# Optimization experiments

Measured on AMD Instinct MI355X. Metric: run time of the kernel, lower is better.

## Reference

```python
import jax, jax.numpy as jnp
import numpy as np

NUM_HEADS = 16
D_K = 64
BATCH_SIZE = 64
NUM_EDGES = 32768


def setup_inputs() -> dict:
    key = jax.random.key(0)
    k1, k2, k3, k4 = jax.random.split(key, 4)
    global_query = jax.random.normal(k1, (NUM_HEADS, BATCH_SIZE, D_K), dtype=jnp.float32)
    local_key = jax.random.normal(k2, (NUM_HEADS, NUM_EDGES, D_K), dtype=jnp.float32)
    local_value = jax.random.normal(k3, (NUM_HEADS, NUM_EDGES, D_K), dtype=jnp.float32)
    batch = jnp.sort(jax.random.randint(k4, (NUM_EDGES,), 0, BATCH_SIZE, dtype=jnp.int64))
    return {"global_query": global_query, "local_key": local_key,
            "local_value": local_value, "batch": batch}


def reference(global_query, local_key, local_value, batch):
    # global_query: [h, b, d]; local_key/value: [h, e, d]; batch: [e] segment ids
    num_heads, batch_size, d_k = global_query.shape
    # seg[b, e] = True iff edge e belongs to graph b
    seg = batch[None, :] == jnp.arange(batch_size, dtype=batch.dtype)[:, None]  # [b, e]
    # NOTE: original module does NOT scale by sqrt(d_k) despite its name
    scores = jnp.einsum('hbd,hed->hbe', global_query, local_key)  # [h, b, e]
    # per-segment softmax: out-of-segment entries get -inf -> exactly 0 weight,
    # matching the original which only softmaxes over edges with batch == i
    masked = jnp.where(seg[None, :, :], scores, -jnp.inf)
    attn = jax.nn.softmax(masked, axis=-1)  # [h, b, e]; zeros outside segment
    output = jnp.einsum('hbe,hed->hbd', attn, local_value)  # [h, b, d]
    return output, attn
```

## Files before the change

### kernel.cpp

```cpp
#include <hip/hip_runtime.h>
#include <math.h>

#define NH 16
#define NB 64
#define DK 64
#define NE 32768

typedef float vf4 __attribute__((ext_vector_type(4)));


__global__ void seg_bounds_kernel(const int* __restrict__ batch, int* __restrict__ bounds) {
    int e = blockIdx.x * 256 + threadIdx.x;
    if (e >= NE) return;
    int be = batch[e];
    if (e == 0) {
        for (int b = 0; b <= be; ++b) bounds[b] = 0;
    } else {
        int bp = batch[e - 1];
        for (int b = bp + 1; b <= be; ++b) bounds[b] = e;
    }
    if (e == NE - 1) {
        for (int b = be + 1; b <= NB; ++b) bounds[b] = NE;
    }
}

__global__ __launch_bounds__(256) void scores_kernel(
    const float* __restrict__ Q,
    const float* __restrict__ K,
    const int*   __restrict__ bounds,
    float* __restrict__ ksc_base,
    float* __restrict__ mstash)
{
    const int g    = blockIdx.x;
    const int task = g >> 1;
    const int half = g & 1;
    const int h    = task >> 6;
    const int b    = task & (NB - 1);
    const int tid  = threadIdx.x;
    const int wave = tid >> 6;
    const int lane = tid & 63;
    const int j    = lane >> 4;
    const int c    = lane & 15;

    const int start = bounds[b];
    const int end   = bounds[b + 1];
    const int S     = end - start;
    const int Sh    = (S + 1) >> 1;
    const int s0    = start + half * Sh;
    const int e1    = (s0 + Sh < end) ? s0 + Sh : end;

    float* ksc = ksc_base + (size_t)h * NE;

    __shared__ float qs[DK];
    __shared__ float sm[4], sl[4];
    if (tid < DK) qs[tid] = Q[((size_t)h * NB + b) * DK + tid];
    __syncthreads();

    const float4 qc = ((const float4*)qs)[c];
    const float4* K4 = (const float4*)(K + (size_t)h * NE * DK);

    float m = -INFINITY, l = 0.f;
    int e = s0 + wave * 4;

    for (; e + 115 < e1; e += 128) {
        float4 kv[8];
        #pragma unroll
        for (int u = 0; u < 8; ++u)
            kv[u] = K4[(size_t)(e + 16 * u + j) * (DK / 4) + c];
        float s[8];
        #pragma unroll
        for (int u = 0; u < 8; ++u) {
            float t = fmaf(kv[u].x, qc.x, fmaf(kv[u].y, qc.y,
                      fmaf(kv[u].z, qc.z, kv[u].w * qc.w)));
            #pragma unroll
            for (int off = 1; off < 16; off <<= 1)
                t += __shfl_xor(t, off);
            s[u] = t;
            if (c == 0) ksc[e + 16 * u + j] = t;
        }
        float mx = fmaxf(fmaxf(fmaxf(s[0], s[1]), fmaxf(s[2], s[3])),
                         fmaxf(fmaxf(s[4], s[5]), fmaxf(s[6], s[7])));
        const float nm = fmaxf(m, mx);
        float sum = 0.f;
        #pragma unroll
        for (int u = 0; u < 8; ++u) sum += __expf(s[u] - nm);
        l = l * __expf(m - nm) + sum;
        m = nm;
    }
    for (; e < e1; e += 16) {
        const int  ej    = e + j;
        const bool valid = ej < e1;
        const int  el    = valid ? ej : e1 - 1;
        const float4 kv = K4[(size_t)el * (DK / 4) + c];
        float s = fmaf(kv.x, qc.x, fmaf(kv.y, qc.y, fmaf(kv.z, qc.z, kv.w * qc.w)));
        #pragma unroll
        for (int off = 1; off < 16; off <<= 1)
            s += __shfl_xor(s, off);
        if (valid) {
            if (c == 0) ksc[ej] = s;
            float nm = fmaxf(m, s);
            l = l * __expf(m - nm) + __expf(s - nm);
            m = nm;
        }
    }

    #pragma unroll
    for (int off = 16; off < 64; off <<= 1) {
        float om = __shfl_xor(m, off);
        float ol = __shfl_xor(l, off);
        float nm = fmaxf(m, om);
        float t1 = (l  > 0.f) ? l  * __expf(m  - nm) : 0.f;
        float t2 = (ol > 0.f) ? ol * __expf(om - nm) : 0.f;
        m = nm; l = t1 + t2;
    }
    if (lane == 0) { sm[wave] = m; sl[wave] = l; }
    __syncthreads();

    if (tid == 0) {
        float M = -INFINITY;
        #pragma unroll
        for (int w = 0; w < 4; ++w) M = fmaxf(M, sm[w]);
        float L = 0.f;
        #pragma unroll
        for (int w = 0; w < 4; ++w) L += (sl[w] > 0.f) ? sl[w] * __expf(sm[w] - M) : 0.f;
        mstash[(task * 2 + half) * 2 + 0] = M;
        mstash[(task * 2 + half) * 2 + 1] = L;
    }
}

__global__ __launch_bounds__(256) void bc_kernel(
    const int*   __restrict__ batch,
    const float* __restrict__ ksc_base,
    const float* __restrict__ mstash,
    const float* __restrict__ V,
    const int*   __restrict__ bounds,
    float* __restrict__ attn,
    float* __restrict__ out)
{
    const int blk = blockIdx.x;
    const int tid = threadIdx.x;
    __shared__ float red[4][16][4];

    if ((blk & 1) == 0) {
        const int wb = blk >> 1;
        const unsigned total = (unsigned)NH * NB * (NE / 4);
        for (unsigned idx = wb * 256u + tid; idx < total; idx += 1024u * 256u) {
            const int e4 = idx & (NE / 4 - 1);
            const int bh = idx >> 13;
            const int b  = bh & (NB - 1);
            const int e0 = e4 << 2;
            const int4 bt = *(const int4*)(batch + e0);
            vf4 r = (vf4)(0.f);
            if (bt.x == b || bt.y == b || bt.z == b || bt.w == b) {
                const float m0 = mstash[bh * 4 + 0], l0 = mstash[bh * 4 + 1];
                const float m1 = mstash[bh * 4 + 2], l1 = mstash[bh * 4 + 3];
                const float M = fmaxf(m0, m1);
                float L = 0.f;
                if (l0 > 0.f) L += l0 * __expf(m0 - M);
                if (l1 > 0.f) L += l1 * __expf(m1 - M);
                const float inv = (L > 0.f) ? 1.f / L : 0.f;
                const int h = bh >> 6;
                const float4 s = *(const float4*)(ksc_base + (size_t)h * NE + e0);
                if (bt.x == b) r.x = __expf(s.x - M) * inv;
                if (bt.y == b) r.y = __expf(s.y - M) * inv;
                if (bt.z == b) r.z = __expf(s.z - M) * inv;
                if (bt.w == b) r.w = __expf(s.w - M) * inv;
            }
            *((vf4*)attn + idx) = r;
        }
    } else {
        const int task = blk >> 1;
        const int h    = task >> 6;
        const int b    = task & (NB - 1);
        const int wave = tid >> 6;
        const int lane = tid & 63;
        const int j    = lane >> 4;
        const int c    = lane & 15;

        const int start = bounds[b];
        const int end   = bounds[b + 1];

        const float m0 = mstash[task * 4 + 0], l0 = mstash[task * 4 + 1];
        const float m1 = mstash[task * 4 + 2], l1 = mstash[task * 4 + 3];
        const float M = fmaxf(m0, m1);
        float L = 0.f;
        if (l0 > 0.f) L += l0 * __expf(m0 - M);
        if (l1 > 0.f) L += l1 * __expf(m1 - M);
        const float inv = (L > 0.f) ? 1.f / L : 0.f;

        const float*  ksc = ksc_base + (size_t)h * NE;
        const float4* V4  = (const float4*)(V + (size_t)h * NE * DK);

        float4 acc = make_float4(0.f, 0.f, 0.f, 0.f);
        int e = start + wave * 4;

        for (; e + 115 < end; e += 128) {
            float4 v[8]; float p[8];
            #pragma unroll
            for (int u = 0; u < 8; ++u) {
                const int ej = e + 16 * u + j;
                p[u] = ksc[ej];
                v[u] = V4[(size_t)ej * (DK / 4) + c];
            }
            #pragma unroll
            for (int u = 0; u < 8; ++u) {
                const float pe = __expf(p[u] - M) * inv;
                acc.x = fmaf(pe, v[u].x, acc.x);
                acc.y = fmaf(pe, v[u].y, acc.y);
                acc.z = fmaf(pe, v[u].z, acc.z);
                acc.w = fmaf(pe, v[u].w, acc.w);
            }
        }
        for (; e < end; e += 16) {
            const int  ej    = e + j;
            const bool valid = ej < end;
            const int  el    = valid ? ej : end - 1;
            const float pe = valid ? __expf(ksc[ej] - M) * inv : 0.f;
            const float4 v = V4[(size_t)el * (DK / 4) + c];
            acc.x = fmaf(pe, v.x, acc.x);
            acc.y = fmaf(pe, v.y, acc.y);
            acc.z = fmaf(pe, v.z, acc.z);
            acc.w = fmaf(pe, v.w, acc.w);
        }

        #pragma unroll
        for (int off = 16; off < 64; off <<= 1) {
            acc.x += __shfl_xor(acc.x, off);
            acc.y += __shfl_xor(acc.y, off);
            acc.z += __shfl_xor(acc.z, off);
            acc.w += __shfl_xor(acc.w, off);
        }
        if (lane < 16) {
            red[wave][c][0] = acc.x;
            red[wave][c][1] = acc.y;
            red[wave][c][2] = acc.z;
            red[wave][c][3] = acc.w;
        }
        __syncthreads();
        if (tid < DK) {
            const int cc = tid >> 2, comp = tid & 3;
            float r = red[0][cc][comp] + red[1][cc][comp]
                    + red[2][cc][comp] + red[3][cc][comp];
            out[((size_t)h * NB + b) * DK + tid] = r;
        }
    }
}

extern "C" void kernel_launch(void* const* d_in, const int* in_sizes, int n_in,
                              void* d_out, int out_size, void* d_ws, size_t ws_size,
                              hipStream_t stream) {
    const float* Q     = (const float*)d_in[0];
    const float* K     = (const float*)d_in[1];
    const float* V     = (const float*)d_in[2];
    const int*   batch = (const int*)d_in[3];

    float* out  = (float*)d_out;
    float* attn = out + (size_t)NH * NB * DK;

    int*   bounds = (int*)d_ws;
    float* ksc    = (float*)d_ws + 128;
    float* mstash = ksc + (size_t)NH * NE;

    seg_bounds_kernel<<<NE / 256, 256, 0, stream>>>(batch, bounds);

    scores_kernel<<<2048, 256, 0, stream>>>(Q, K, bounds, ksc, mstash);

    bc_kernel<<<2048, 256, 0, stream>>>(batch, ksc, mstash, V, bounds, attn, out);
}
```

Before: 330.8 us.

## Fuse scores, softmax, attn write and PV into one kernel per head-segment

Merges the scores and the attn/output kernels into one kernel with one block per (head, graph), keeping each segment's scores in LDS instead of a global scratch buffer. Every block writes its full attention row, with zeros outside its segment, plus the normalized probabilities and the weighted V sum. This removes one launch and the global score round trip, and it no longer scans the batch array for the attn fill. In exchange the grid shrinks from 2048 to 1024 blocks with no split of a segment across two blocks, and segments longer than the LDS capacity fall back to recomputing the scores.

```diff
diff --git a/kernel.cpp b/kernel.cpp
--- a/kernel.cpp
+++ b/kernel.cpp
@@ -5,6 +5,7 @@
 #define NB 64
 #define DK 64
 #define NE 32768
+#define LDS_CAP 2048
 
 typedef float vf4 __attribute__((ext_vector_type(4)));
 
@@ -24,16 +25,15 @@
     }
 }
 
-__global__ __launch_bounds__(256) void scores_kernel(
+__global__ __launch_bounds__(256) void fused_kernel(
     const float* __restrict__ Q,
     const float* __restrict__ K,
+    const float* __restrict__ V,
     const int*   __restrict__ bounds,
-    float* __restrict__ ksc_base,
-    float* __restrict__ mstash)
+    float* __restrict__ out,
+    float* __restrict__ attn)
 {
-    const int g    = blockIdx.x;
-    const int task = g >> 1;
-    const int half = g & 1;
+    const int task = blockIdx.x;
     const int h    = task >> 6;
     const int b    = task & (NB - 1);
     const int tid  = threadIdx.x;
@@ -45,24 +45,25 @@
     const int start = bounds[b];
     const int end   = bounds[b + 1];
     const int S     = end - start;
-    const int Sh    = (S + 1) >> 1;
-    const int s0    = start + half * Sh;
-    const int e1    = (s0 + Sh < end) ? s0 + Sh : end;
-
-    float* ksc = ksc_base + (size_t)h * NE;
+    const bool single = (S <= LDS_CAP);
 
     __shared__ float qs[DK];
+    __shared__ float ssc[LDS_CAP];
     __shared__ float sm[4], sl[4];
+    __shared__ float bM, bInv;
+    __shared__ float red[4][16][4];
+
     if (tid < DK) qs[tid] = Q[((size_t)h * NB + b) * DK + tid];
     __syncthreads();
 
-    const float4 qc = ((const float4*)qs)[c];
-    const float4* K4 = (const float4*)(K + (size_t)h * NE * DK);
+    const float4  qc  = ((const float4*)qs)[c];
+    const float4* K4  = (const float4*)(K + (size_t)h * NE * DK);
+    const float4* V4  = (const float4*)(V + (size_t)h * NE * DK);
+    float* arow = attn + ((size_t)h * NB + b) * NE;
 
     float m = -INFINITY, l = 0.f;
-    int e = s0 + wave * 4;
-
-    for (; e + 115 < e1; e += 128) {
+    int e = start + wave * 4;
+    for (; e + 115 < end; e += 128) {
         float4 kv[8];
         #pragma unroll
         for (int u = 0; u < 8; ++u)
@@ -76,7 +77,7 @@
             for (int off = 1; off < 16; off <<= 1)
                 t += __shfl_xor(t, off);
             s[u] = t;
-            if (c == 0) ksc[e + 16 * u + j] = t;
+            if (single && c == 0) ssc[e + 16 * u + j - start] = t;
         }
         float mx = fmaxf(fmaxf(fmaxf(s[0], s[1]), fmaxf(s[2], s[3])),
                          fmaxf(fmaxf(s[4], s[5]), fmaxf(s[6], s[7])));
@@ -87,19 +88,19 @@
         l = l * __expf(m - nm) + sum;
         m = nm;
     }
-    for (; e < e1; e += 16) {
+    for (; e < end; e += 16) {
         const int  ej    = e + j;
-        const bool valid = ej < e1;
-        const int  el    = valid ? ej : e1 - 1;
+        const bool valid = ej < end;
+        const int  el    = valid ? ej : end - 1;
         const float4 kv = K4[(size_t)el * (DK / 4) + c];
-        float s = fmaf(kv.x, qc.x, fmaf(kv.y, qc.y, fmaf(kv.z, qc.z, kv.w * qc.w)));
+        float t = fmaf(kv.x, qc.x, fmaf(kv.y, qc.y, fmaf(kv.z, qc.z, kv.w * qc.w)));
         #pragma unroll
         for (int off = 1; off < 16; off <<= 1)
-            s += __shfl_xor(s, off);
+            t += __shfl_xor(t, off);
         if (valid) {
-            if (c == 0) ksc[ej] = s;
-            float nm = fmaxf(m, s);
-            l = l * __expf(m - nm) + __expf(s - nm);
+            if (single && c == 0) ssc[ej - start] = t;
+            float nm = fmaxf(m, t);
+            l = l * __expf(m - nm) + __expf(t - nm);
             m = nm;
         }
     }
@@ -115,7 +116,6 @@
     }
     if (lane == 0) { sm[wave] = m; sl[wave] = l; }
     __syncthreads();
-
     if (tid == 0) {
         float M = -INFINITY;
         #pragma unroll
@@ -123,83 +123,39 @@
         float L = 0.f;
         #pragma unroll
         for (int w = 0; w < 4; ++w) L += (sl[w] > 0.f) ? sl[w] * __expf(sm[w] - M) : 0.f;
-        mstash[(task * 2 + half) * 2 + 0] = M;
-        mstash[(task * 2 + half) * 2 + 1] = L;
-    }
-}
-
-__global__ __launch_bounds__(256) void bc_kernel(
-    const int*   __restrict__ batch,
-    const float* __restrict__ ksc_base,
-    const float* __restrict__ mstash,
-    const float* __restrict__ V,
-    const int*   __restrict__ bounds,
-    float* __restrict__ attn,
-    float* __restrict__ out)
-{
-    const int blk = blockIdx.x;
-    const int tid = threadIdx.x;
-    __shared__ float red[4][16][4];
-
-    if ((blk & 1) == 0) {
-        const int wb = blk >> 1;
-        const unsigned total = (unsigned)NH * NB * (NE / 4);
-        for (unsigned idx = wb * 256u + tid; idx < total; idx += 1024u * 256u) {
-            const int e4 = idx & (NE / 4 - 1);
-            const int bh = idx >> 13;
-            const int b  = bh & (NB - 1);
-            const int e0 = e4 << 2;
-            const int4 bt = *(const int4*)(batch + e0);
-            vf4 r = (vf4)(0.f);
-            if (bt.x == b || bt.y == b || bt.z == b || bt.w == b) {
-                const float m0 = mstash[bh * 4 + 0], l0 = mstash[bh * 4 + 1];
-                const float m1 = mstash[bh * 4 + 2], l1 = mstash[bh * 4 + 3];
-                const float M = fmaxf(m0, m1);
-                float L = 0.f;
-                if (l0 > 0.f) L += l0 * __expf(m0 - M);
-                if (l1 > 0.f) L += l1 * __expf(m1 - M);
-                const float inv = (L > 0.f) ? 1.f / L : 0.f;
-                const int h = bh >> 6;
-                const float4 s = *(const float4*)(ksc_base + (size_t)h * NE + e0);
-                if (bt.x == b) r.x = __expf(s.x - M) * inv;
-                if (bt.y == b) r.y = __expf(s.y - M) * inv;
-                if (bt.z == b) r.z = __expf(s.z - M) * inv;
-                if (bt.w == b) r.w = __expf(s.w - M) * inv;
-            }
-            *((vf4*)attn + idx) = r;
-        }
-    } else {
-        const int task = blk >> 1;
-        const int h    = task >> 6;
-        const int b    = task & (NB - 1);
-        const int wave = tid >> 6;
-        const int lane = tid & 63;
-        const int j    = lane >> 4;
-        const int c    = lane & 15;
-
-        const int start = bounds[b];
-        const int end   = bounds[b + 1];
-
-        const float m0 = mstash[task * 4 + 0], l0 = mstash[task * 4 + 1];
-        const float m1 = mstash[task * 4 + 2], l1 = mstash[task * 4 + 3];
-        const float M = fmaxf(m0, m1);
-        float L = 0.f;
-        if (l0 > 0.f) L += l0 * __expf(m0 - M);
-        if (l1 > 0.f) L += l1 * __expf(m1 - M);
-        const float inv = (L > 0.f) ? 1.f / L : 0.f;
-
-        const float*  ksc = ksc_base + (size_t)h * NE;
-        const float4* V4  = (const float4*)(V + (size_t)h * NE * DK);
-
-        float4 acc = make_float4(0.f, 0.f, 0.f, 0.f);
-        int e = start + wave * 4;
-
-        for (; e + 115 < end; e += 128) {
+        bM = M; bInv = (L > 0.f) ? 1.f / L : 0.f;
+    }
+    __syncthreads();
+    const float M   = bM;
+    const float inv = bInv;
+
+    {
+        vf4 z4 = (vf4)(0.f);
+        vf4* arow4 = (vf4*)arow;
+        const int zs = start >> 2;
+        const int ze = (end + 3) >> 2;
+        for (int i = tid; i < zs; i += 256) arow4[i] = z4;
+        for (int i = ze + tid; i < NE / 4; i += 256) arow4[i] = z4;
+        if (tid == 0) {
+            for (int p = (zs << 2); p < start; ++p) arow[p] = 0.f;
+        } else if (tid == 1) {
+            for (int p = end; p < (ze << 2); ++p) arow[p] = 0.f;
+        }
+    }
+
+    float4 acc = make_float4(0.f, 0.f, 0.f, 0.f);
+
+    if (single) {
+        for (int ep = start + tid; ep < end; ep += 256)
+            arow[ep] = __expf(ssc[ep - start] - M) * inv;
+
+        int ev = start + wave * 4;
+        for (; ev + 115 < end; ev += 128) {
             float4 v[8]; float p[8];
             #pragma unroll
             for (int u = 0; u < 8; ++u) {
-                const int ej = e + 16 * u + j;
-                p[u] = ksc[ej];
+                const int ej = ev + 16 * u + j;
+                p[u] = ssc[ej - start];
                 v[u] = V4[(size_t)ej * (DK / 4) + c];
             }
             #pragma unroll
@@ -211,38 +167,68 @@
                 acc.w = fmaf(pe, v[u].w, acc.w);
             }
         }
-        for (; e < end; e += 16) {
-            const int  ej    = e + j;
+        for (; ev < end; ev += 16) {
+            const int  ej    = ev + j;
             const bool valid = ej < end;
             const int  el    = valid ? ej : end - 1;
-            const float pe = valid ? __expf(ksc[ej] - M) * inv : 0.f;
+            const float pe = valid ? __expf(ssc[el - start] - M) * inv : 0.f;
             const float4 v = V4[(size_t)el * (DK / 4) + c];
             acc.x = fmaf(pe, v.x, acc.x);
             acc.y = fmaf(pe, v.y, acc.y);
             acc.z = fmaf(pe, v.z, acc.z);
             acc.w = fmaf(pe, v.w, acc.w);
         }
-
-        #pragma unroll
-        for (int off = 16; off < 64; off <<= 1) {
-            acc.x += __shfl_xor(acc.x, off);
-            acc.y += __shfl_xor(acc.y, off);
-            acc.z += __shfl_xor(acc.z, off);
-            acc.w += __shfl_xor(acc.w, off);
-        }
-        if (lane < 16) {
-            red[wave][c][0] = acc.x;
-            red[wave][c][1] = acc.y;
-            red[wave][c][2] = acc.z;
-            red[wave][c][3] = acc.w;
-        }
-        __syncthreads();
-        if (tid < DK) {
-            const int cc = tid >> 2, comp = tid & 3;
-            float r = red[0][cc][comp] + red[1][cc][comp]
-                    + red[2][cc][comp] + red[3][cc][comp];
-            out[((size_t)h * NB + b) * DK + tid] = r;
-        }
+    } else {
+        for (int cs = start; cs < end; cs += LDS_CAP) {
+            const int ce = (cs + LDS_CAP < end) ? cs + LDS_CAP : end;
+            __syncthreads();
+            for (int ek = cs + wave * 4; ek < ce; ek += 16) {
+                const int  ej    = ek + j;
+                const bool valid = ej < ce;
+                const int  el    = valid ? ej : ce - 1;
+                const float4 kv = K4[(size_t)el * (DK / 4) + c];
+                float t = fmaf(kv.x, qc.x, fmaf(kv.y, qc.y, fmaf(kv.z, qc.z, kv.w * qc.w)));
+                #pragma unroll
+                for (int off = 1; off < 16; off <<= 1)
+                    t += __shfl_xor(t, off);
+                if (valid && c == 0) ssc[el - cs] = t;
+            }
+            __syncthreads();
+            for (int ep = cs + tid; ep < ce; ep += 256)
+                arow[ep] = __expf(ssc[ep - cs] - M) * inv;
+            for (int ev = cs + wave * 4; ev < ce; ev += 16) {
+                const int  ej    = ev + j;
+                const bool valid = ej < ce;
+                const int  el    = valid ? ej : ce - 1;
+                const float pe = valid ? __expf(ssc[el - cs] - M) * inv : 0.f;
+                const float4 v = V4[(size_t)el * (DK / 4) + c];
+                acc.x = fmaf(pe, v.x, acc.x);
+                acc.y = fmaf(pe, v.y, acc.y);
+                acc.z = fmaf(pe, v.z, acc.z);
+                acc.w = fmaf(pe, v.w, acc.w);
+            }
+        }
+    }
+
+    #pragma unroll
+    for (int off = 16; off < 64; off <<= 1) {
+        acc.x += __shfl_xor(acc.x, off);
+        acc.y += __shfl_xor(acc.y, off);
+        acc.z += __shfl_xor(acc.z, off);
+        acc.w += __shfl_xor(acc.w, off);
+    }
+    if (lane < 16) {
+        red[wave][c][0] = acc.x;
+        red[wave][c][1] = acc.y;
+        red[wave][c][2] = acc.z;
+        red[wave][c][3] = acc.w;
+    }
+    __syncthreads();
+    if (tid < DK) {
+        const int cc = tid >> 2, comp = tid & 3;
+        float r = red[0][cc][comp] + red[1][cc][comp]
+                + red[2][cc][comp] + red[3][cc][comp];
+        out[((size_t)h * NB + b) * DK + tid] = r;
     }
 }
 
@@ -258,12 +244,8 @@
     float* attn = out + (size_t)NH * NB * DK;
 
     int*   bounds = (int*)d_ws;
-    float* ksc    = (float*)d_ws + 128;
-    float* mstash = ksc + (size_t)NH * NE;
 
     seg_bounds_kernel<<<NE / 256, 256, 0, stream>>>(batch, bounds);
 
-    scores_kernel<<<2048, 256, 0, stream>>>(Q, K, bounds, ksc, mstash);
-
-    bc_kernel<<<2048, 256, 0, stream>>>(batch, ksc, mstash, V, bounds, attn, out);
+    fused_kernel<<<NH * NB, 256, 0, stream>>>(Q, K, V, bounds, out, attn);
 }
```

Measured after the change: 324.2 us. -2.0%, faster.
